# Optimization experiments

Hardware: AMD Instinct MI355X
Metric: run time of the kernel (lower is better)

The kernel has to match this reference:

```python
import jax, jax.numpy as jnp
import numpy as np

NUM_HEADS = 32
NUM_KV_HEADS = 8
HEAD_DIM = 128


def setup_inputs() -> dict:
    key = jax.random.key(0)
    ks = jax.random.split(key, 5)
    B, S, H = 2, 2048, 4096
    Dq = NUM_HEADS * HEAD_DIM      # 4096
    Dkv = NUM_KV_HEADS * HEAD_DIM  # 1024
    return {
        "hidden_states": jax.random.normal(ks[0], (B, S, H), jnp.float32),
        "w_q": jax.random.normal(ks[1], (H, Dq), jnp.float32) * 0.02,
        "w_k": jax.random.normal(ks[2], (H, Dkv), jnp.float32) * 0.02,
        "w_v": jax.random.normal(ks[3], (H, Dkv), jnp.float32) * 0.02,
        "w_o": jax.random.normal(ks[4], (Dq, H), jnp.float32) * 0.02,
    }


def reference(hidden_states, w_q, w_k, w_v, w_o):
    # GQA causal attention, prefill path (no KV cache, RoPE is a no-op in source).
    B, S, _ = hidden_states.shape
    Hq, Hkv, D = NUM_HEADS, NUM_KV_HEADS, HEAD_DIM
    g = Hq // Hkv  # kv groups
    scale = D ** -0.5

    q = (hidden_states @ w_q).reshape(B, S, Hkv, g, D)  # [B,S,Hkv,g,D]
    k = (hidden_states @ w_k).reshape(B, S, Hkv, D)     # [B,S,Hkv,D]
    v = (hidden_states @ w_v).reshape(B, S, Hkv, D)

    # repeat_kv expressed as grouped einsum (avoids materializing repeated K/V)
    scores = jnp.einsum('bqhgd,bkhd->bhgqk', q, k) * scale  # [B,Hkv,g,S,S]
    causal = jnp.tril(jnp.ones((S, S), dtype=bool))
    scores = jnp.where(causal, scores, -jnp.inf)
    probs = jax.nn.softmax(scores.astype(jnp.float32), axis=-1).astype(q.dtype)

    attn = jnp.einsum('bhgqk,bkhd->bqhgd', probs, v)  # [B,S,Hkv,g,D]
    attn = attn.reshape(B, S, Hq * D)
    return attn @ w_o
```

## Files before the change

kernel.cpp:

```cpp
#include <hip/hip_runtime.h>

typedef unsigned short u16;
typedef __attribute__((ext_vector_type(8))) short bf16x8;
typedef __attribute__((ext_vector_type(8))) unsigned short u16x8;
typedef __attribute__((ext_vector_type(4))) unsigned short u16x4;
typedef __attribute__((ext_vector_type(4))) float f32x4;

__device__ __forceinline__ u16 f2bf(float f) {
  union { float f; unsigned u; } v; v.f = f;
  unsigned r = v.u + 0x7fffu + ((v.u >> 16) & 1u);
  return (u16)(r >> 16);
}

__device__ __forceinline__ void gload16(const u16* g, u16* l) {
  __builtin_amdgcn_global_load_lds((const __attribute__((address_space(1))) void*)g,
                                   (__attribute__((address_space(3))) void*)l, 16, 0, 0);
}

__global__ __launch_bounds__(256) void cast_bf16_kern(const float* __restrict__ in,
                                                      u16* __restrict__ out, int n) {
  int i = (blockIdx.x * 256 + threadIdx.x) * 8;
  if (i >= n) return;
  float4 a = *(const float4*)(in + i);
  float4 b = *(const float4*)(in + i + 4);
  u16x8 r;
  r[0] = f2bf(a.x); r[1] = f2bf(a.y); r[2] = f2bf(a.z); r[3] = f2bf(a.w);
  r[4] = f2bf(b.x); r[5] = f2bf(b.y); r[6] = f2bf(b.z); r[7] = f2bf(b.w);
  *(u16x8*)(out + i) = r;
}

__global__ __launch_bounds__(256) void transpose_cast_kern(const float* __restrict__ in,
                                                           u16* __restrict__ out, int K, int N) {
  __shared__ float tile[64][65];
  int nbx = N >> 6;
  int n0 = (blockIdx.x % nbx) << 6;
  int k0 = (blockIdx.x / nbx) << 6;
  int tx = threadIdx.x & 15;
  int ty = threadIdx.x >> 4;
#pragma unroll
  for (int r = 0; r < 64; r += 16) {
    float4 v = *(const float4*)(in + (size_t)(k0 + ty + r) * N + n0 + tx * 4);
    tile[ty + r][tx * 4 + 0] = v.x;
    tile[ty + r][tx * 4 + 1] = v.y;
    tile[ty + r][tx * 4 + 2] = v.z;
    tile[ty + r][tx * 4 + 3] = v.w;
  }
  __syncthreads();
#pragma unroll
  for (int r = 0; r < 64; r += 16) {
    u16x4 o;
#pragma unroll
    for (int j = 0; j < 4; j++) o[j] = f2bf(tile[tx * 4 + j][ty + r]);
    *(u16x4*)(out + (size_t)(n0 + ty + r) * K + k0 + tx * 4) = o;
  }
}

template <int MODE>
__global__ __launch_bounds__(256) void gemm_bt(const u16* __restrict__ A,
                                               const u16* __restrict__ Bt,
                                               void* __restrict__ Cout,
                                               void* __restrict__ Cout2,
                                               int M, int N, int K) {
  __shared__ u16 As[128 * 32];
  __shared__ u16 Bs[128 * 32];
  const int tid = threadIdx.x;
  const int lane = tid & 63, wv = tid >> 6;
  const int wr = wv >> 1, wc = wv & 1;
  const int li = lane & 15, lg = lane >> 4;
  const int nbx = N >> 7;
  const int m0 = (blockIdx.x / nbx) << 7;
  const int n0 = (blockIdx.x % nbx) << 7;

  f32x4 acc[4][4];
#pragma unroll
  for (int m = 0; m < 4; m++)
#pragma unroll
    for (int n = 0; n < 4; n++) acc[m][n] = (f32x4){0.f, 0.f, 0.f, 0.f};

  const int srow = wv * 16 + (lane >> 2);
  const int skoff = (lane & 3) * 8;
  const u16* ag0 = A + (size_t)(m0 + srow) * K + skoff;
  const u16* ag1 = A + (size_t)(m0 + srow + 64) * K + skoff;
  const u16* bg0 = Bt + (size_t)(n0 + srow) * K + skoff;
  const u16* bg1 = Bt + (size_t)(n0 + srow + 64) * K + skoff;
  u16* al = As + wv * 512;
  u16* bl = Bs + wv * 512;

  for (int kt = 0; kt < K; kt += 32) {
    __syncthreads();
    gload16(ag0 + kt, al);
    gload16(ag1 + kt, al + 2048);
    gload16(bg0 + kt, bl);
    gload16(bg1 + kt, bl + 2048);
    __syncthreads();
    bf16x8 af[4], bfr[4];
#pragma unroll
    for (int m = 0; m < 4; m++)
      af[m] = *(const bf16x8*)(As + (wr * 64 + m * 16 + li) * 32 + lg * 8);
#pragma unroll
    for (int n = 0; n < 4; n++)
      bfr[n] = *(const bf16x8*)(Bs + (wc * 64 + n * 16 + li) * 32 + lg * 8);
#pragma unroll
    for (int m = 0; m < 4; m++)
#pragma unroll
      for (int n = 0; n < 4; n++)
        acc[m][n] = __builtin_amdgcn_mfma_f32_16x16x32_bf16(af[m], bfr[n], acc[m][n], 0, 0, 0);
  }

#pragma unroll
  for (int m = 0; m < 4; m++)
#pragma unroll
    for (int n = 0; n < 4; n++)
#pragma unroll
      for (int r = 0; r < 4; r++) {
        int gm = m0 + wr * 64 + m * 16 + lg * 4 + r;
        int gn = n0 + wc * 64 + n * 16 + li;
        float val = acc[m][n][r];
        if (MODE == 0) {
          ((u16*)Cout)[(size_t)gm * N + gn] = f2bf(val);
        } else {
          if (gn < 1024) {
            ((u16*)Cout)[(size_t)gm * 1024 + gn] = f2bf(val);
          } else {
            int c = gn - 1024;
            int b = gm >> 11, s = gm & 2047, kvh = c >> 7, d = c & 127;
            int s2 = (s & ~31) | (((s >> 2) & 3) << 3) | (((s >> 4) & 1) << 2) | (s & 3);
            ((u16*)Cout2)[(size_t)((b * 8 + kvh) * 128 + d) * 2048 + s2] = f2bf(val);
          }
        }
      }
}

#define PH_PRE()                                           \
  asm volatile("" ::: "memory");                           \
  __builtin_amdgcn_s_barrier();                            \
  asm volatile("s_waitcnt lgkmcnt(0)" ::: "memory");       \
  __builtin_amdgcn_sched_barrier(0);                       \
  __builtin_amdgcn_s_setprio(1)

#define PH_POST()                                          \
  __builtin_amdgcn_s_setprio(0);                           \
  __builtin_amdgcn_sched_barrier(0);                       \
  asm volatile("" ::: "memory");                           \
  __builtin_amdgcn_s_barrier()

template <int MODE>
__global__ __launch_bounds__(512, 2) void gemm256(const u16* __restrict__ A,
                                                  const u16* __restrict__ Bt,
                                                  void* __restrict__ Cout,
                                                  int M, int N, int K) {
  __shared__ u16 lds[65536];
  const int tid = threadIdx.x;
  const int lane = tid & 63, w = tid >> 6;
  const int wm = w >> 2, wn = w & 3;
  const int li = lane & 15, lg = lane >> 4;
  const int NT = K >> 6;

  const int nbx = N >> 8;
  const int nwg = gridDim.x;
  const int swz = (blockIdx.x & 7) * (nwg >> 3) + (blockIdx.x >> 3);
  const int m0 = (swz / nbx) << 8;
  const int n0 = (swz % nbx) << 8;

  const int srow = w * 16 + (lane >> 3);
  const int scol = ((lane & 7) ^ (lane >> 3)) << 3;
  const u16* sA0 = A + (size_t)(m0 + srow) * K + scol;
  const u16* sA1 = A + (size_t)(m0 + 128 + srow) * K + scol;
  const u16* sB0 = Bt + (size_t)(n0 + srow) * K + scol;
  const u16* sB1 = Bt + (size_t)(n0 + 128 + srow) * K + scol;
  const size_t jK = (size_t)8 * K;
  u16* dA0 = lds + w * 1024;
  u16* dA1 = lds + 8192 + w * 1024;
  u16* dB0 = lds + 32768 + w * 1024;
  u16* dB1 = lds + 32768 + 8192 + w * 1024;

#define STG(sp, dp, t_) do {                                          \
    int db_ = (t_) & 1;                                               \
    gload16((sp) + (size_t)(t_) * 64, (dp) + db_ * 16384);            \
    gload16((sp) + (size_t)(t_) * 64 + jK, (dp) + db_ * 16384 + 512); \
  } while (0)

  STG(sA0, dA0, 0); STG(sA1, dA1, 0); STG(sB0, dB0, 0); STG(sB1, dB1, 0);
  STG(sA0, dA0, 1); STG(sA1, dA1, 1); STG(sB0, dB0, 1); STG(sB1, dB1, 1);
  asm volatile("s_waitcnt vmcnt(8)" ::: "memory");
  asm volatile("" ::: "memory");
  __builtin_amdgcn_s_barrier();

  f32x4 acc[8][4];
#pragma unroll
  for (int m = 0; m < 8; m++)
#pragma unroll
    for (int n = 0; n < 4; n++) acc[m][n] = (f32x4){0.f, 0.f, 0.f, 0.f};

  const int xsw = (li & 7) << 3;
  const int k0o = (lg * 8) ^ xsw;
  const int k1o = (32 + lg * 8) ^ xsw;
  const u16* aBase = lds + wm * 8192;
  const u16* bBase = lds + 32768 + (wn >> 1) * 8192;
  const int brow0 = (wn & 1) * 64;

  bf16x8 a[4][2], b[4][2];

  for (int t = 0; t < NT; ++t) {
    const int db = t & 1;
    const u16* Ab = aBase + db * 16384;
    const u16* Bb = bBase + db * 16384;

#pragma unroll
    for (int mf = 0; mf < 4; mf++) {
      int r = mf * 16 + li;
      a[mf][0] = *(const bf16x8*)(Ab + r * 64 + k0o);
      a[mf][1] = *(const bf16x8*)(Ab + r * 64 + k1o);
    }
#pragma unroll
    for (int nf = 0; nf < 2; nf++) {
      int r = brow0 + nf * 16 + li;
      b[nf][0] = *(const bf16x8*)(Bb + r * 64 + k0o);
      b[nf][1] = *(const bf16x8*)(Bb + r * 64 + k1o);
    }
    asm volatile("s_waitcnt lgkmcnt(8)" ::: "memory");
    PH_PRE();
#pragma unroll
    for (int mf = 0; mf < 4; mf++)
#pragma unroll
      for (int nf = 0; nf < 2; nf++) {
        acc[mf][nf] = __builtin_amdgcn_mfma_f32_16x16x32_bf16(a[mf][0], b[nf][0], acc[mf][nf], 0, 0, 0);
        acc[mf][nf] = __builtin_amdgcn_mfma_f32_16x16x32_bf16(a[mf][1], b[nf][1], acc[mf][nf], 0, 0, 0);
      }
    PH_POST();

#pragma unroll
    for (int nf = 2; nf < 4; nf++) {
      int r = brow0 + nf * 16 + li;
      b[nf][0] = *(const bf16x8*)(Bb + r * 64 + k0o);
      b[nf][1] = *(const bf16x8*)(Bb + r * 64 + k1o);
    }
    PH_PRE();
#pragma unroll
    for (int mf = 0; mf < 4; mf++)
#pragma unroll
      for (int nf = 2; nf < 4; nf++) {
        acc[mf][nf] = __builtin_amdgcn_mfma_f32_16x16x32_bf16(a[mf][0], b[nf][0], acc[mf][nf], 0, 0, 0);
        acc[mf][nf] = __builtin_amdgcn_mfma_f32_16x16x32_bf16(a[mf][1], b[nf][1], acc[mf][nf], 0, 0, 0);
      }
    PH_POST();

#pragma unroll
    for (int mf = 0; mf < 4; mf++) {
      int r = (mf + 4) * 16 + li;
      a[mf][0] = *(const bf16x8*)(Ab + r * 64 + k0o);
      a[mf][1] = *(const bf16x8*)(Ab + r * 64 + k1o);
    }
    if (t + 2 < NT) { STG(sB0, dB0, t + 2); STG(sB1, dB1, t + 2); }
    asm volatile("s_waitcnt lgkmcnt(4)" ::: "memory");
    PH_PRE();
#pragma unroll
    for (int mf = 0; mf < 4; mf++)
#pragma unroll
      for (int nf = 2; nf < 4; nf++) {
        acc[mf + 4][nf] = __builtin_amdgcn_mfma_f32_16x16x32_bf16(a[mf][0], b[nf][0], acc[mf + 4][nf], 0, 0, 0);
        acc[mf + 4][nf] = __builtin_amdgcn_mfma_f32_16x16x32_bf16(a[mf][1], b[nf][1], acc[mf + 4][nf], 0, 0, 0);
      }
    PH_POST();

    if (t + 2 < NT) { STG(sA0, dA0, t + 2); STG(sA1, dA1, t + 2); }
    PH_PRE();
#pragma unroll
    for (int mf = 0; mf < 4; mf++)
#pragma unroll
      for (int nf = 0; nf < 2; nf++) {
        acc[mf + 4][nf] = __builtin_amdgcn_mfma_f32_16x16x32_bf16(a[mf][0], b[nf][0], acc[mf + 4][nf], 0, 0, 0);
        acc[mf + 4][nf] = __builtin_amdgcn_mfma_f32_16x16x32_bf16(a[mf][1], b[nf][1], acc[mf + 4][nf], 0, 0, 0);
      }
    __builtin_amdgcn_s_setprio(0);
    __builtin_amdgcn_sched_barrier(0);
    if (t < NT - 2) {
      asm volatile("s_waitcnt vmcnt(8)" ::: "memory");
    } else {
      asm volatile("s_waitcnt vmcnt(0)" ::: "memory");
    }
    asm volatile("" ::: "memory");
    __builtin_amdgcn_s_barrier();
  }

#pragma unroll
  for (int mf = 0; mf < 8; mf++)
#pragma unroll
    for (int nf = 0; nf < 4; nf++)
#pragma unroll
      for (int r = 0; r < 4; r++) {
        int gm = m0 + wm * 128 + mf * 16 + lg * 4 + r;
        int gn = n0 + wn * 64 + nf * 16 + li;
        if (MODE == 0)
          ((u16*)Cout)[(size_t)gm * N + gn] = f2bf(acc[mf][nf][r]);
        else
          ((float*)Cout)[(size_t)gm * N + gn] = acc[mf][nf][r];
      }
#undef STG
}

__global__ __launch_bounds__(256, 2) void flash_attn_kern(const u16* __restrict__ Qg,
                                                          const u16* __restrict__ Kg,
                                                          const u16* __restrict__ VT,
                                                          u16* __restrict__ Og) {
  const int bid = blockIdx.x;
  const int qt = 63 - (bid >> 4);
  const int gh = bid & 15;
  const int b = gh >> 3, kvh = gh & 7;
  const int tid = threadIdx.x;
  const int lane = tid & 63, w = tid >> 6;
  const int li = lane & 15, lg = lane >> 4;
  const int h = kvh * 4 + w;
  const int q0 = qt << 5;
  const int nt = (qt >> 1) + 1;

  __shared__ u16 Kbuf[2][8192];
  __shared__ u16 Vbuf[2][8192];

  bf16x8 qf[2][4];
  {
    const u16* qp = Qg + ((size_t)(b * 2048 + q0 + li)) * 4096 + h * 128 + lg * 8;
#pragma unroll
    for (int m = 0; m < 2; m++)
#pragma unroll
      for (int ks = 0; ks < 4; ks++)
        qf[m][ks] = *(const bf16x8*)(qp + (size_t)(m * 16) * 4096 + ks * 32);
  }

  const u16* ksrc[4];
  const u16* vsrc[4];
#pragma unroll
  for (int i = 0; i < 4; i++) {
    int c = w * 4 + i;
    int krow = c * 4 + (lane >> 4);
    int kinner = ((lane & 15) * 16) ^ ((krow & 7) << 4);
    ksrc[i] = Kg + (size_t)(b * 2048 + krow) * 1024 + kvh * 128 + (kinner >> 1);
    int vrow = c * 8 + (lane >> 3);
    int vinner = ((lane & 7) * 16) ^ ((vrow & 7) << 4);
    vsrc[i] = VT + (size_t)((b * 8 + kvh) * 128 + vrow) * 2048 + (vinner >> 1);
  }
#pragma unroll
  for (int i = 0; i < 4; i++) {
    int c = w * 4 + i;
    gload16(ksrc[i], &Kbuf[0][c * 512]);
    gload16(vsrc[i], &Vbuf[0][c * 512]);
    ksrc[i] += 64 * 1024;
    vsrc[i] += 64;
  }

  f32x4 oa[2][8];
#pragma unroll
  for (int m = 0; m < 2; m++)
#pragma unroll
    for (int n = 0; n < 8; n++) oa[m][n] = (f32x4){0.f, 0.f, 0.f, 0.f};
  f32x4 lacc[2];
  lacc[0] = (f32x4){0.f, 0.f, 0.f, 0.f};
  lacc[1] = (f32x4){0.f, 0.f, 0.f, 0.f};
  float mrun[2] = {-1e30f, -1e30f};

  const float scale = 0.08838834764831845f;
  bf16x8 onesf;
#pragma unroll
  for (int j = 0; j < 8; j++) onesf[j] = (short)0x3F80;

  asm volatile("s_waitcnt vmcnt(0)\n\ts_barrier" ::: "memory");

  for (int t = 0; t < nt; ++t) {
    const int cur = t & 1;
    const u16* KB = Kbuf[cur];
    const u16* VB = Vbuf[cur];
    if (t + 1 < nt) {
#pragma unroll
      for (int i = 0; i < 4; i++) {
        int c = w * 4 + i;
        gload16(ksrc[i], &Kbuf[cur ^ 1][c * 512]);
        gload16(vsrc[i], &Vbuf[cur ^ 1][c * 512]);
        ksrc[i] += 64 * 1024;
        vsrc[i] += 64;
      }
    }

    f32x4 sacc[2][4];
#pragma unroll
    for (int m = 0; m < 2; m++)
#pragma unroll
      for (int n = 0; n < 4; n++) sacc[m][n] = (f32x4){0.f, 0.f, 0.f, 0.f};
    __builtin_amdgcn_s_setprio(1);
#pragma unroll
    for (int n = 0; n < 4; n++) {
      int krow = n * 16 + li;
      const u16* kb = KB + krow * 128;
      int sw = (krow & 7) << 4;
#pragma unroll
      for (int ks = 0; ks < 4; ks++) {
        bf16x8 kf = *(const bf16x8*)(kb + (((ks * 64 + lg * 16) ^ sw) >> 1));
        sacc[0][n] = __builtin_amdgcn_mfma_f32_16x16x32_bf16(kf, qf[0][ks], sacc[0][n], 0, 0, 0);
        sacc[1][n] = __builtin_amdgcn_mfma_f32_16x16x32_bf16(kf, qf[1][ks], sacc[1][n], 0, 0, 0);
      }
    }
    __builtin_amdgcn_s_setprio(0);

#pragma unroll
    for (int m = 0; m < 2; m++)
#pragma unroll
      for (int n = 0; n < 4; n++)
#pragma unroll
        for (int r = 0; r < 4; r++) sacc[m][n][r] *= scale;
    if (t == nt - 1) {
      const int kv0 = t * 64;
#pragma unroll
      for (int m = 0; m < 2; m++) {
        int q = q0 + m * 16 + li;
#pragma unroll
        for (int n = 0; n < 4; n++)
#pragma unroll
          for (int r = 0; r < 4; r++)
            if (kv0 + n * 16 + lg * 4 + r > q) sacc[m][n][r] = -1e30f;
      }
    }

#pragma unroll
    for (int m = 0; m < 2; m++) {
      float mx = sacc[m][0][0];
#pragma unroll
      for (int n = 0; n < 4; n++)
#pragma unroll
        for (int r = 0; r < 4; r++) mx = fmaxf(mx, sacc[m][n][r]);
      mx = fmaxf(mx, __shfl_xor(mx, 16, 64));
      mx = fmaxf(mx, __shfl_xor(mx, 32, 64));
      float mnew = fmaxf(mrun[m], mx);
      float corr = __expf(mrun[m] - mnew);
      mrun[m] = mnew;
#pragma unroll
      for (int n = 0; n < 4; n++)
#pragma unroll
        for (int r = 0; r < 4; r++) sacc[m][n][r] = __expf(sacc[m][n][r] - mnew);
#pragma unroll
      for (int r = 0; r < 4; r++) lacc[m][r] *= corr;
#pragma unroll
      for (int n = 0; n < 8; n++)
#pragma unroll
        for (int r = 0; r < 4; r++) oa[m][n][r] *= corr;
    }

    bf16x8 pf[2][2];
#pragma unroll
    for (int m = 0; m < 2; m++)
#pragma unroll
      for (int kvs = 0; kvs < 2; kvs++) {
        u16x8 pw;
#pragma unroll
        for (int e = 0; e < 8; e++) pw[e] = f2bf(sacc[m][2 * kvs + (e >> 2)][e & 3]);
        pf[m][kvs] = *(bf16x8*)&pw;
      }

    __builtin_amdgcn_s_setprio(1);
#pragma unroll
    for (int kvs = 0; kvs < 2; kvs++) {
#pragma unroll
      for (int n = 0; n < 8; n++) {
        int vrow = n * 16 + li;
        bf16x8 vf = *(const bf16x8*)(VB + vrow * 64 +
                                     (((kvs * 64 + lg * 16) ^ ((vrow & 7) << 4)) >> 1));
        oa[0][n] = __builtin_amdgcn_mfma_f32_16x16x32_bf16(vf, pf[0][kvs], oa[0][n], 0, 0, 0);
        oa[1][n] = __builtin_amdgcn_mfma_f32_16x16x32_bf16(vf, pf[1][kvs], oa[1][n], 0, 0, 0);
      }
      lacc[0] = __builtin_amdgcn_mfma_f32_16x16x32_bf16(onesf, pf[0][kvs], lacc[0], 0, 0, 0);
      lacc[1] = __builtin_amdgcn_mfma_f32_16x16x32_bf16(onesf, pf[1][kvs], lacc[1], 0, 0, 0);
    }
    __builtin_amdgcn_s_setprio(0);

    asm volatile("s_waitcnt vmcnt(0)\n\ts_barrier" ::: "memory");
  }

#pragma unroll
  for (int m = 0; m < 2; m++) {
    float inv = 1.0f / lacc[m][0];
    u16* op = Og + (size_t)(b * 2048 + q0 + m * 16 + li) * 4096 + h * 128 + lg * 4;
#pragma unroll
    for (int n = 0; n < 8; n++) {
      u16x4 o;
#pragma unroll
      for (int r = 0; r < 4; r++) o[r] = f2bf(oa[m][n][r] * inv);
      *(u16x4*)(op + n * 16) = o;
    }
  }
}

extern "C" void kernel_launch(void* const* d_in, const int* in_sizes, int n_in,
                              void* d_out, int out_size, void* d_ws, size_t ws_size,
                              hipStream_t stream) {
  (void)in_sizes; (void)n_in; (void)out_size; (void)ws_size;
  const float* hs = (const float*)d_in[0];
  const float* wq = (const float*)d_in[1];
  const float* wk = (const float*)d_in[2];
  const float* wv = (const float*)d_in[3];
  const float* wo = (const float*)d_in[4];

  u16* ws   = (u16*)d_ws;
  u16* hs_b = ws;
  u16* wqT  = hs_b + 16777216;
  u16* wkT  = wqT + 16777216;
  u16* wvT  = wkT + 4194304;
  u16* woT  = wvT + 4194304;
  u16* Qb   = woT + 16777216;
  u16* Kb   = Qb + 16777216;
  u16* VTb  = Kb + 4194304;
  u16* attnb = VTb + 4194304;

  cast_bf16_kern<<<8192, 256, 0, stream>>>(hs, hs_b, 16777216);
  transpose_cast_kern<<<4096, 256, 0, stream>>>(wq, wqT, 4096, 4096);
  transpose_cast_kern<<<1024, 256, 0, stream>>>(wk, wkT, 4096, 1024);
  transpose_cast_kern<<<1024, 256, 0, stream>>>(wv, wvT, 4096, 1024);
  transpose_cast_kern<<<4096, 256, 0, stream>>>(wo, woT, 4096, 4096);

  gemm256<0><<<256, 512, 0, stream>>>(hs_b, wqT, Qb, 4096, 4096, 4096);
  gemm_bt<3><<<512, 256, 0, stream>>>(hs_b, wkT, Kb, VTb, 4096, 2048, 4096);

  flash_attn_kern<<<1024, 256, 0, stream>>>(Qb, Kb, VTb, attnb);

  gemm256<2><<<256, 512, 0, stream>>>(attnb, woT, (float*)d_out, 4096, 4096, 4096);
}
```

Measured before the change: 517.0 us.

## Replace simple K/V GEMM with pipelined 128x256 swizzled-LDS kernel; relax gemm256 sync

Replaces the naive single-buffered gemm_bt used for the fused K/V projection with a new gemm_kv kernel. The new kernel uses 512 threads, double-buffered direct-to-LDS loads with XOR swizzle, staged prefetch, and setprio-phased MFMA blocks. This aims to hide global load latency and LDS bank conflicts in that projection. It also removes explicit lgkmcnt waits and sched_barriers from the gemm256 phase macros, leaving LDS read ordering to the compiler. That may change scheduling, and correctness now depends on the compiler inserting the right waits.

Result: faster. 482.0 us, median of 2 (-6.8%).

```diff
diff --git a/kernel.cpp b/kernel.cpp
--- a/kernel.cpp
+++ b/kernel.cpp
@@ -55,94 +55,17 @@
   }
 }
 
-template <int MODE>
-__global__ __launch_bounds__(256) void gemm_bt(const u16* __restrict__ A,
-                                               const u16* __restrict__ Bt,
-                                               void* __restrict__ Cout,
-                                               void* __restrict__ Cout2,
-                                               int M, int N, int K) {
-  __shared__ u16 As[128 * 32];
-  __shared__ u16 Bs[128 * 32];
-  const int tid = threadIdx.x;
-  const int lane = tid & 63, wv = tid >> 6;
-  const int wr = wv >> 1, wc = wv & 1;
-  const int li = lane & 15, lg = lane >> 4;
-  const int nbx = N >> 7;
-  const int m0 = (blockIdx.x / nbx) << 7;
-  const int n0 = (blockIdx.x % nbx) << 7;
-
-  f32x4 acc[4][4];
-#pragma unroll
-  for (int m = 0; m < 4; m++)
-#pragma unroll
-    for (int n = 0; n < 4; n++) acc[m][n] = (f32x4){0.f, 0.f, 0.f, 0.f};
-
-  const int srow = wv * 16 + (lane >> 2);
-  const int skoff = (lane & 3) * 8;
-  const u16* ag0 = A + (size_t)(m0 + srow) * K + skoff;
-  const u16* ag1 = A + (size_t)(m0 + srow + 64) * K + skoff;
-  const u16* bg0 = Bt + (size_t)(n0 + srow) * K + skoff;
-  const u16* bg1 = Bt + (size_t)(n0 + srow + 64) * K + skoff;
-  u16* al = As + wv * 512;
-  u16* bl = Bs + wv * 512;
-
-  for (int kt = 0; kt < K; kt += 32) {
-    __syncthreads();
-    gload16(ag0 + kt, al);
-    gload16(ag1 + kt, al + 2048);
-    gload16(bg0 + kt, bl);
-    gload16(bg1 + kt, bl + 2048);
-    __syncthreads();
-    bf16x8 af[4], bfr[4];
-#pragma unroll
-    for (int m = 0; m < 4; m++)
-      af[m] = *(const bf16x8*)(As + (wr * 64 + m * 16 + li) * 32 + lg * 8);
-#pragma unroll
-    for (int n = 0; n < 4; n++)
-      bfr[n] = *(const bf16x8*)(Bs + (wc * 64 + n * 16 + li) * 32 + lg * 8);
-#pragma unroll
-    for (int m = 0; m < 4; m++)
-#pragma unroll
-      for (int n = 0; n < 4; n++)
-        acc[m][n] = __builtin_amdgcn_mfma_f32_16x16x32_bf16(af[m], bfr[n], acc[m][n], 0, 0, 0);
-  }
-
-#pragma unroll
-  for (int m = 0; m < 4; m++)
-#pragma unroll
-    for (int n = 0; n < 4; n++)
-#pragma unroll
-      for (int r = 0; r < 4; r++) {
-        int gm = m0 + wr * 64 + m * 16 + lg * 4 + r;
-        int gn = n0 + wc * 64 + n * 16 + li;
-        float val = acc[m][n][r];
-        if (MODE == 0) {
-          ((u16*)Cout)[(size_t)gm * N + gn] = f2bf(val);
-        } else {
-          if (gn < 1024) {
-            ((u16*)Cout)[(size_t)gm * 1024 + gn] = f2bf(val);
-          } else {
-            int c = gn - 1024;
-            int b = gm >> 11, s = gm & 2047, kvh = c >> 7, d = c & 127;
-            int s2 = (s & ~31) | (((s >> 2) & 3) << 3) | (((s >> 4) & 1) << 2) | (s & 3);
-            ((u16*)Cout2)[(size_t)((b * 8 + kvh) * 128 + d) * 2048 + s2] = f2bf(val);
-          }
-        }
-      }
-}
-
 #define PH_PRE()                                           \
   asm volatile("" ::: "memory");                           \
   __builtin_amdgcn_s_barrier();                            \
-  asm volatile("s_waitcnt lgkmcnt(0)" ::: "memory");       \
-  __builtin_amdgcn_sched_barrier(0);                       \
+  asm volatile("" ::: "memory");                           \
   __builtin_amdgcn_s_setprio(1)
 
 #define PH_POST()                                          \
   __builtin_amdgcn_s_setprio(0);                           \
-  __builtin_amdgcn_sched_barrier(0);                       \
   asm volatile("" ::: "memory");                           \
-  __builtin_amdgcn_s_barrier()
+  __builtin_amdgcn_s_barrier();                            \
+  asm volatile("" ::: "memory")
 
 template <int MODE>
 __global__ __launch_bounds__(512, 2) void gemm256(const u16* __restrict__ A,
@@ -183,8 +106,8 @@
   STG(sA0, dA0, 0); STG(sA1, dA1, 0); STG(sB0, dB0, 0); STG(sB1, dB1, 0);
   STG(sA0, dA0, 1); STG(sA1, dA1, 1); STG(sB0, dB0, 1); STG(sB1, dB1, 1);
   asm volatile("s_waitcnt vmcnt(8)" ::: "memory");
+  __builtin_amdgcn_s_barrier();
   asm volatile("" ::: "memory");
-  __builtin_amdgcn_s_barrier();
 
   f32x4 acc[8][4];
 #pragma unroll
@@ -218,7 +141,6 @@
       b[nf][0] = *(const bf16x8*)(Bb + r * 64 + k0o);
       b[nf][1] = *(const bf16x8*)(Bb + r * 64 + k1o);
     }
-    asm volatile("s_waitcnt lgkmcnt(8)" ::: "memory");
     PH_PRE();
 #pragma unroll
     for (int mf = 0; mf < 4; mf++)
@@ -252,7 +174,6 @@
       a[mf][1] = *(const bf16x8*)(Ab + r * 64 + k1o);
     }
     if (t + 2 < NT) { STG(sB0, dB0, t + 2); STG(sB1, dB1, t + 2); }
-    asm volatile("s_waitcnt lgkmcnt(4)" ::: "memory");
     PH_PRE();
 #pragma unroll
     for (int mf = 0; mf < 4; mf++)
@@ -273,14 +194,13 @@
         acc[mf + 4][nf] = __builtin_amdgcn_mfma_f32_16x16x32_bf16(a[mf][1], b[nf][1], acc[mf + 4][nf], 0, 0, 0);
       }
     __builtin_amdgcn_s_setprio(0);
-    __builtin_amdgcn_sched_barrier(0);
     if (t < NT - 2) {
       asm volatile("s_waitcnt vmcnt(8)" ::: "memory");
     } else {
       asm volatile("s_waitcnt vmcnt(0)" ::: "memory");
     }
+    __builtin_amdgcn_s_barrier();
     asm volatile("" ::: "memory");
-    __builtin_amdgcn_s_barrier();
   }
 
 #pragma unroll
@@ -297,6 +217,135 @@
           ((float*)Cout)[(size_t)gm * N + gn] = acc[mf][nf][r];
       }
 #undef STG
+}
+
+__global__ __launch_bounds__(512, 2) void gemm_kv(const u16* __restrict__ A,
+                                                  const u16* __restrict__ Bt,
+                                                  u16* __restrict__ Kout,
+                                                  u16* __restrict__ Vout) {
+  __shared__ u16 lds[49152];
+  const int tid = threadIdx.x;
+  const int lane = tid & 63, w = tid >> 6;
+  const int wm = w >> 2, wn = w & 3;
+  const int li = lane & 15, lg = lane >> 4;
+  const int K = 4096, NT = 64;
+
+  const int swz = (blockIdx.x & 7) * 32 + (blockIdx.x >> 3);
+  const int m0 = (swz >> 3) << 7;
+  const int n0 = (swz & 7) << 8;
+
+  const int srow = w * 16 + (lane >> 3);
+  const int scol = ((lane & 7) ^ (lane >> 3)) << 3;
+  const u16* sA  = A  + (size_t)(m0 + srow) * K + scol;
+  const u16* sB0 = Bt + (size_t)(n0 + srow) * K + scol;
+  const u16* sB1 = Bt + (size_t)(n0 + 128 + srow) * K + scol;
+  const size_t jK = (size_t)8 * K;
+  u16* dA  = lds + w * 1024;
+  u16* dB0 = lds + 16384 + w * 1024;
+  u16* dB1 = lds + 16384 + 8192 + w * 1024;
+
+#define STGA(t_) do { int db_ = (t_) & 1;                                     \
+    gload16(sA + (size_t)(t_) * 64, dA + db_ * 8192);                         \
+    gload16(sA + (size_t)(t_) * 64 + jK, dA + db_ * 8192 + 512); } while (0)
+#define STGB(t_) do { int db_ = (t_) & 1;                                     \
+    gload16(sB0 + (size_t)(t_) * 64, dB0 + db_ * 16384);                      \
+    gload16(sB0 + (size_t)(t_) * 64 + jK, dB0 + db_ * 16384 + 512);           \
+    gload16(sB1 + (size_t)(t_) * 64, dB1 + db_ * 16384);                      \
+    gload16(sB1 + (size_t)(t_) * 64 + jK, dB1 + db_ * 16384 + 512); } while (0)
+
+  STGA(0); STGB(0); STGB(1);
+  asm volatile("s_waitcnt vmcnt(4)" ::: "memory");
+  __builtin_amdgcn_s_barrier();
+  asm volatile("" ::: "memory");
+
+  f32x4 acc[4][4];
+#pragma unroll
+  for (int m = 0; m < 4; m++)
+#pragma unroll
+    for (int n = 0; n < 4; n++) acc[m][n] = (f32x4){0.f, 0.f, 0.f, 0.f};
+
+  const int xsw = (li & 7) << 3;
+  const int k0o = (lg * 8) ^ xsw;
+  const int k1o = (32 + lg * 8) ^ xsw;
+  const int arow0 = wm * 64;
+  const u16* bBase0 = lds + 16384 + (wn >> 1) * 8192;
+  const int brow0 = (wn & 1) * 64;
+
+  bf16x8 a[4][2], b[4][2];
+
+  for (int t = 0; t < NT; ++t) {
+    const int db = t & 1;
+    const u16* Ab = lds + db * 8192;
+    const u16* Bb = bBase0 + db * 16384;
+
+#pragma unroll
+    for (int mf = 0; mf < 2; mf++) {
+      int r = arow0 + mf * 16 + li;
+      a[mf][0] = *(const bf16x8*)(Ab + r * 64 + k0o);
+      a[mf][1] = *(const bf16x8*)(Ab + r * 64 + k1o);
+    }
+#pragma unroll
+    for (int nf = 0; nf < 4; nf++) {
+      int r = brow0 + nf * 16 + li;
+      b[nf][0] = *(const bf16x8*)(Bb + r * 64 + k0o);
+      b[nf][1] = *(const bf16x8*)(Bb + r * 64 + k1o);
+    }
+    if (t + 1 < NT) STGA(t + 1);
+    PH_PRE();
+#pragma unroll
+    for (int mf = 0; mf < 2; mf++)
+#pragma unroll
+      for (int nf = 0; nf < 4; nf++) {
+        acc[mf][nf] = __builtin_amdgcn_mfma_f32_16x16x32_bf16(a[mf][0], b[nf][0], acc[mf][nf], 0, 0, 0);
+        acc[mf][nf] = __builtin_amdgcn_mfma_f32_16x16x32_bf16(a[mf][1], b[nf][1], acc[mf][nf], 0, 0, 0);
+      }
+    PH_POST();
+
+#pragma unroll
+    for (int mf = 2; mf < 4; mf++) {
+      int r = arow0 + mf * 16 + li;
+      a[mf][0] = *(const bf16x8*)(Ab + r * 64 + k0o);
+      a[mf][1] = *(const bf16x8*)(Ab + r * 64 + k1o);
+    }
+    if (t + 2 < NT) STGB(t + 2);
+    PH_PRE();
+#pragma unroll
+    for (int mf = 2; mf < 4; mf++)
+#pragma unroll
+      for (int nf = 0; nf < 4; nf++) {
+        acc[mf][nf] = __builtin_amdgcn_mfma_f32_16x16x32_bf16(a[mf][0], b[nf][0], acc[mf][nf], 0, 0, 0);
+        acc[mf][nf] = __builtin_amdgcn_mfma_f32_16x16x32_bf16(a[mf][1], b[nf][1], acc[mf][nf], 0, 0, 0);
+      }
+    __builtin_amdgcn_s_setprio(0);
+    if (t < NT - 2) {
+      asm volatile("s_waitcnt vmcnt(4)" ::: "memory");
+    } else {
+      asm volatile("s_waitcnt vmcnt(0)" ::: "memory");
+    }
+    __builtin_amdgcn_s_barrier();
+    asm volatile("" ::: "memory");
+  }
+
+#pragma unroll
+  for (int mf = 0; mf < 4; mf++)
+#pragma unroll
+    for (int nf = 0; nf < 4; nf++)
+#pragma unroll
+      for (int r = 0; r < 4; r++) {
+        int gm = m0 + wm * 64 + mf * 16 + lg * 4 + r;
+        int gn = n0 + wn * 64 + nf * 16 + li;
+        float val = acc[mf][nf][r];
+        if (gn < 1024) {
+          Kout[(size_t)gm * 1024 + gn] = f2bf(val);
+        } else {
+          int c = gn - 1024;
+          int b = gm >> 11, s = gm & 2047, kvh = c >> 7, d = c & 127;
+          int s2 = (s & ~31) | (((s >> 2) & 3) << 3) | (((s >> 4) & 1) << 2) | (s & 3);
+          Vout[(size_t)((b * 8 + kvh) * 128 + d) * 2048 + s2] = f2bf(val);
+        }
+      }
+#undef STGA
+#undef STGB
 }
 
 __global__ __launch_bounds__(256, 2) void flash_attn_kern(const u16* __restrict__ Qg,
@@ -515,7 +564,7 @@
   transpose_cast_kern<<<4096, 256, 0, stream>>>(wo, woT, 4096, 4096);
 
   gemm256<0><<<256, 512, 0, stream>>>(hs_b, wqT, Qb, 4096, 4096, 4096);
-  gemm_bt<3><<<512, 256, 0, stream>>>(hs_b, wkT, Kb, VTb, 4096, 2048, 4096);
+  gemm_kv<<<256, 512, 0, stream>>>(hs_b, wkT, Kb, VTb);
 
   flash_attn_kern<<<1024, 256, 0, stream>>>(Qb, Kb, VTb, attnb);
 
```

## Fuse QKV projections into one gemm256 launch and merge prep kernels

Applied to the files above, without the earlier changes.

Merges the five cast/transpose kernels into a single prep kernel dispatched by block index. Replaces the separate Q GEMM and the simpler 128-tile K/V GEMM with one 256-tile gemm256 over N=6144. This works because wqT, wkT and wvT sit contiguously in the workspace, and a new epilogue mode routes columns to Q, K and the swizzled V-transpose buffer. It also drops the explicit lgkmcnt waits and sched_barriers in the MFMA phases, leaving LDS wait placement to the compiler. The aim is fewer launches, better efficiency for the K/V projection, and a fuller grid, at the cost of a branchier epilogue and less hand control over scheduling.

New measurement: 524.1 us. No clear change (+1.4%).

```diff
diff --git a/kernel.cpp b/kernel.cpp
--- a/kernel.cpp
+++ b/kernel.cpp
@@ -17,24 +17,12 @@
                                    (__attribute__((address_space(3))) void*)l, 16, 0, 0);
 }
 
-__global__ __launch_bounds__(256) void cast_bf16_kern(const float* __restrict__ in,
-                                                      u16* __restrict__ out, int n) {
-  int i = (blockIdx.x * 256 + threadIdx.x) * 8;
-  if (i >= n) return;
-  float4 a = *(const float4*)(in + i);
-  float4 b = *(const float4*)(in + i + 4);
-  u16x8 r;
-  r[0] = f2bf(a.x); r[1] = f2bf(a.y); r[2] = f2bf(a.z); r[3] = f2bf(a.w);
-  r[4] = f2bf(b.x); r[5] = f2bf(b.y); r[6] = f2bf(b.z); r[7] = f2bf(b.w);
-  *(u16x8*)(out + i) = r;
-}
-
-__global__ __launch_bounds__(256) void transpose_cast_kern(const float* __restrict__ in,
-                                                           u16* __restrict__ out, int K, int N) {
-  __shared__ float tile[64][65];
+__device__ __forceinline__ void transpose_body(const float* __restrict__ in,
+                                               u16* __restrict__ out, int K, int N,
+                                               int bid, float (*tile)[65]) {
   int nbx = N >> 6;
-  int n0 = (blockIdx.x % nbx) << 6;
-  int k0 = (blockIdx.x / nbx) << 6;
+  int n0 = (bid % nbx) << 6;
+  int k0 = (bid / nbx) << 6;
   int tx = threadIdx.x & 15;
   int ty = threadIdx.x >> 4;
 #pragma unroll
@@ -55,99 +43,55 @@
   }
 }
 
-template <int MODE>
-__global__ __launch_bounds__(256) void gemm_bt(const u16* __restrict__ A,
-                                               const u16* __restrict__ Bt,
-                                               void* __restrict__ Cout,
-                                               void* __restrict__ Cout2,
-                                               int M, int N, int K) {
-  __shared__ u16 As[128 * 32];
-  __shared__ u16 Bs[128 * 32];
-  const int tid = threadIdx.x;
-  const int lane = tid & 63, wv = tid >> 6;
-  const int wr = wv >> 1, wc = wv & 1;
-  const int li = lane & 15, lg = lane >> 4;
-  const int nbx = N >> 7;
-  const int m0 = (blockIdx.x / nbx) << 7;
-  const int n0 = (blockIdx.x % nbx) << 7;
-
-  f32x4 acc[4][4];
-#pragma unroll
-  for (int m = 0; m < 4; m++)
-#pragma unroll
-    for (int n = 0; n < 4; n++) acc[m][n] = (f32x4){0.f, 0.f, 0.f, 0.f};
-
-  const int srow = wv * 16 + (lane >> 2);
-  const int skoff = (lane & 3) * 8;
-  const u16* ag0 = A + (size_t)(m0 + srow) * K + skoff;
-  const u16* ag1 = A + (size_t)(m0 + srow + 64) * K + skoff;
-  const u16* bg0 = Bt + (size_t)(n0 + srow) * K + skoff;
-  const u16* bg1 = Bt + (size_t)(n0 + srow + 64) * K + skoff;
-  u16* al = As + wv * 512;
-  u16* bl = Bs + wv * 512;
-
-  for (int kt = 0; kt < K; kt += 32) {
-    __syncthreads();
-    gload16(ag0 + kt, al);
-    gload16(ag1 + kt, al + 2048);
-    gload16(bg0 + kt, bl);
-    gload16(bg1 + kt, bl + 2048);
-    __syncthreads();
-    bf16x8 af[4], bfr[4];
-#pragma unroll
-    for (int m = 0; m < 4; m++)
-      af[m] = *(const bf16x8*)(As + (wr * 64 + m * 16 + li) * 32 + lg * 8);
-#pragma unroll
-    for (int n = 0; n < 4; n++)
-      bfr[n] = *(const bf16x8*)(Bs + (wc * 64 + n * 16 + li) * 32 + lg * 8);
-#pragma unroll
-    for (int m = 0; m < 4; m++)
-#pragma unroll
-      for (int n = 0; n < 4; n++)
-        acc[m][n] = __builtin_amdgcn_mfma_f32_16x16x32_bf16(af[m], bfr[n], acc[m][n], 0, 0, 0);
-  }
-
-#pragma unroll
-  for (int m = 0; m < 4; m++)
-#pragma unroll
-    for (int n = 0; n < 4; n++)
-#pragma unroll
-      for (int r = 0; r < 4; r++) {
-        int gm = m0 + wr * 64 + m * 16 + lg * 4 + r;
-        int gn = n0 + wc * 64 + n * 16 + li;
-        float val = acc[m][n][r];
-        if (MODE == 0) {
-          ((u16*)Cout)[(size_t)gm * N + gn] = f2bf(val);
-        } else {
-          if (gn < 1024) {
-            ((u16*)Cout)[(size_t)gm * 1024 + gn] = f2bf(val);
-          } else {
-            int c = gn - 1024;
-            int b = gm >> 11, s = gm & 2047, kvh = c >> 7, d = c & 127;
-            int s2 = (s & ~31) | (((s >> 2) & 3) << 3) | (((s >> 4) & 1) << 2) | (s & 3);
-            ((u16*)Cout2)[(size_t)((b * 8 + kvh) * 128 + d) * 2048 + s2] = f2bf(val);
-          }
-        }
-      }
+__global__ __launch_bounds__(256) void prep_kern(const float* __restrict__ hs,
+                                                 const float* __restrict__ wq,
+                                                 const float* __restrict__ wk,
+                                                 const float* __restrict__ wv,
+                                                 const float* __restrict__ wo,
+                                                 u16* __restrict__ hs_b,
+                                                 u16* __restrict__ wqT,
+                                                 u16* __restrict__ wkT,
+                                                 u16* __restrict__ wvT,
+                                                 u16* __restrict__ woT) {
+  __shared__ float tile[64][65];
+  int b = blockIdx.x;
+  if (b < 8192) {
+    int i = (b * 256 + threadIdx.x) * 8;
+    float4 a = *(const float4*)(hs + i);
+    float4 c = *(const float4*)(hs + i + 4);
+    u16x8 r;
+    r[0] = f2bf(a.x); r[1] = f2bf(a.y); r[2] = f2bf(a.z); r[3] = f2bf(a.w);
+    r[4] = f2bf(c.x); r[5] = f2bf(c.y); r[6] = f2bf(c.z); r[7] = f2bf(c.w);
+    *(u16x8*)(hs_b + i) = r;
+  } else if (b < 12288) {
+    transpose_body(wq, wqT, 4096, 4096, b - 8192, tile);
+  } else if (b < 13312) {
+    transpose_body(wk, wkT, 4096, 1024, b - 12288, tile);
+  } else if (b < 14336) {
+    transpose_body(wv, wvT, 4096, 1024, b - 13312, tile);
+  } else {
+    transpose_body(wo, woT, 4096, 4096, b - 14336, tile);
+  }
 }
 
 #define PH_PRE()                                           \
   asm volatile("" ::: "memory");                           \
   __builtin_amdgcn_s_barrier();                            \
-  asm volatile("s_waitcnt lgkmcnt(0)" ::: "memory");       \
-  __builtin_amdgcn_sched_barrier(0);                       \
+  asm volatile("" ::: "memory");                           \
   __builtin_amdgcn_s_setprio(1)
 
 #define PH_POST()                                          \
   __builtin_amdgcn_s_setprio(0);                           \
-  __builtin_amdgcn_sched_barrier(0);                       \
   asm volatile("" ::: "memory");                           \
-  __builtin_amdgcn_s_barrier()
+  __builtin_amdgcn_s_barrier();                            \
+  asm volatile("" ::: "memory")
 
 template <int MODE>
 __global__ __launch_bounds__(512, 2) void gemm256(const u16* __restrict__ A,
                                                   const u16* __restrict__ Bt,
                                                   void* __restrict__ Cout,
+                                                  void* __restrict__ C2,
+                                                  void* __restrict__ C3,
                                                   int M, int N, int K) {
   __shared__ u16 lds[65536];
   const int tid = threadIdx.x;
@@ -183,8 +127,8 @@
   STG(sA0, dA0, 0); STG(sA1, dA1, 0); STG(sB0, dB0, 0); STG(sB1, dB1, 0);
   STG(sA0, dA0, 1); STG(sA1, dA1, 1); STG(sB0, dB0, 1); STG(sB1, dB1, 1);
   asm volatile("s_waitcnt vmcnt(8)" ::: "memory");
+  __builtin_amdgcn_s_barrier();
   asm volatile("" ::: "memory");
-  __builtin_amdgcn_s_barrier();
 
   f32x4 acc[8][4];
 #pragma unroll
@@ -218,7 +162,6 @@
       b[nf][0] = *(const bf16x8*)(Bb + r * 64 + k0o);
       b[nf][1] = *(const bf16x8*)(Bb + r * 64 + k1o);
     }
-    asm volatile("s_waitcnt lgkmcnt(8)" ::: "memory");
     PH_PRE();
 #pragma unroll
     for (int mf = 0; mf < 4; mf++)
@@ -252,7 +195,6 @@
       a[mf][1] = *(const bf16x8*)(Ab + r * 64 + k1o);
     }
     if (t + 2 < NT) { STG(sB0, dB0, t + 2); STG(sB1, dB1, t + 2); }
-    asm volatile("s_waitcnt lgkmcnt(4)" ::: "memory");
     PH_PRE();
 #pragma unroll
     for (int mf = 0; mf < 4; mf++)
@@ -273,14 +215,13 @@
         acc[mf + 4][nf] = __builtin_amdgcn_mfma_f32_16x16x32_bf16(a[mf][1], b[nf][1], acc[mf + 4][nf], 0, 0, 0);
       }
     __builtin_amdgcn_s_setprio(0);
-    __builtin_amdgcn_sched_barrier(0);
     if (t < NT - 2) {
       asm volatile("s_waitcnt vmcnt(8)" ::: "memory");
     } else {
       asm volatile("s_waitcnt vmcnt(0)" ::: "memory");
     }
+    __builtin_amdgcn_s_barrier();
     asm volatile("" ::: "memory");
-    __builtin_amdgcn_s_barrier();
   }
 
 #pragma unroll
@@ -291,10 +232,24 @@
       for (int r = 0; r < 4; r++) {
         int gm = m0 + wm * 128 + mf * 16 + lg * 4 + r;
         int gn = n0 + wn * 64 + nf * 16 + li;
-        if (MODE == 0)
-          ((u16*)Cout)[(size_t)gm * N + gn] = f2bf(acc[mf][nf][r]);
-        else
-          ((float*)Cout)[(size_t)gm * N + gn] = acc[mf][nf][r];
+        float val = acc[mf][nf][r];
+        if (MODE == 0) {
+          ((u16*)Cout)[(size_t)gm * N + gn] = f2bf(val);
+        } else if (MODE == 2) {
+          ((float*)Cout)[(size_t)gm * N + gn] = val;
+        } else {
+          if (gn < 4096) {
+            ((u16*)Cout)[(size_t)gm * 4096 + gn] = f2bf(val);
+          } else if (gn < 5120) {
+            int c = gn - 4096;
+            ((u16*)C2)[(size_t)gm * 1024 + c] = f2bf(val);
+          } else {
+            int c = gn - 5120;
+            int bb = gm >> 11, s = gm & 2047, kvh = c >> 7, d = c & 127;
+            int s2 = (s & ~31) | (((s >> 2) & 3) << 3) | (((s >> 4) & 1) << 2) | (s & 3);
+            ((u16*)C3)[(size_t)((bb * 8 + kvh) * 128 + d) * 2048 + s2] = f2bf(val);
+          }
+        }
       }
 #undef STG
 }
@@ -508,16 +463,12 @@
   u16* VTb  = Kb + 4194304;
   u16* attnb = VTb + 4194304;
 
-  cast_bf16_kern<<<8192, 256, 0, stream>>>(hs, hs_b, 16777216);
-  transpose_cast_kern<<<4096, 256, 0, stream>>>(wq, wqT, 4096, 4096);
-  transpose_cast_kern<<<1024, 256, 0, stream>>>(wk, wkT, 4096, 1024);
-  transpose_cast_kern<<<1024, 256, 0, stream>>>(wv, wvT, 4096, 1024);
-  transpose_cast_kern<<<4096, 256, 0, stream>>>(wo, woT, 4096, 4096);
-
-  gemm256<0><<<256, 512, 0, stream>>>(hs_b, wqT, Qb, 4096, 4096, 4096);
-  gemm_bt<3><<<512, 256, 0, stream>>>(hs_b, wkT, Kb, VTb, 4096, 2048, 4096);
+  prep_kern<<<18432, 256, 0, stream>>>(hs, wq, wk, wv, wo, hs_b, wqT, wkT, wvT, woT);
+
+  gemm256<3><<<384, 512, 0, stream>>>(hs_b, wqT, Qb, Kb, VTb, 4096, 6144, 4096);
 
   flash_attn_kern<<<1024, 256, 0, stream>>>(Qb, Kb, VTb, attnb);
 
-  gemm256<2><<<256, 512, 0, stream>>>(attnb, woT, (float*)d_out, 4096, 4096, 4096);
-}
+  gemm256<2><<<256, 512, 0, stream>>>(attnb, woT, (float*)d_out, nullptr, nullptr,
+                                      4096, 4096, 4096);
+}
```
